# Performance work log

Measured on AMD Instinct MI355X. Metric: run time of the kernel, lower is better.

Reference implementation:

```python
import jax, jax.numpy as jnp
import numpy as np

B, C, L = 64, 64, 8192
EPS = float(np.finfo(np.float32).eps)  # matches np.finfo(np.float32).eps in the torch code


def setup_inputs() -> dict:
    key = jax.random.key(0)
    k1, k2, k3 = jax.random.split(key, 3)
    data = jax.random.normal(k1, (B, C, L), dtype=jnp.float32)
    idxes = jax.random.randint(k2, (B, L), 0, L).astype(jnp.int32)
    # prefix lengths in [1, L] so every slice is non-empty (ragged branch)
    zero_pos = jax.random.randint(k3, (B,), 1, L + 1)
    return {"data": data, "idxes": idxes, "zero_pos": zero_pos}


def reference(data, idxes, zero_pos):
    # data: [B, C, L]; per-batch mean/std over the prefix data[b, :, :zero_pos[b]]
    Bn, Cn, Ln = data.shape
    mask = (jnp.arange(Ln)[None, :] < zero_pos[:, None])[:, None, :].astype(data.dtype)  # [B,1,L]
    cnt = Cn * zero_pos.astype(data.dtype)  # [B] number of elements in each prefix
    mean = jnp.sum(data * mask, axis=(1, 2)) / cnt  # [B]
    diff = (data - mean[:, None, None]) * mask  # [B,C,L]
    var = jnp.sum(diff * diff, axis=(1, 2)) / (cnt - 1.0)  # unbiased, as torch.std
    std = jnp.sqrt(var)  # [B]
    out = (data - mean[:, None, None]) / (std[:, None, None] + EPS)
    return (out, idxes, zero_pos)
```

## Files before the change

kernel.cpp:

```cpp
#include <hip/hip_runtime.h>
#include <hip/hip_bf16.h>
#include <math.h>

#define BB 64
#define CC 64
#define LL 8192
#define EPS_F 1.1920928955078125e-07f
#define STATS_SPLITS 16


__global__ void tln_stats(const float* __restrict__ data,
                          const int* __restrict__ zero_pos,
                          float* __restrict__ sums) {
    const int b = blockIdx.x;
    const int s = blockIdx.y;
    const int tid = threadIdx.x;
    const int zp = zero_pos[b];
    const int nv = zp >> 2;
    const float* base = data + (size_t)b * CC * LL;

    float sum = 0.0f, sq = 0.0f;
    for (int c = s; c < CC; c += STATS_SPLITS) {
        const float* rowp = base + (size_t)c * LL;
        const float4* row4 = (const float4*)rowp;
        for (int i = tid; i < nv; i += 256) {
            float4 v = row4[i];
            sum += v.x + v.y + v.z + v.w;
            sq  += v.x * v.x + v.y * v.y + v.z * v.z + v.w * v.w;
        }
        for (int l = (nv << 2) + tid; l < zp; l += 256) {
            float v = rowp[l];
            sum += v;
            sq  += v * v;
        }
    }

    #pragma unroll
    for (int off = 32; off > 0; off >>= 1) {
        sum += __shfl_down(sum, off);
        sq  += __shfl_down(sq, off);
    }
    __shared__ float lsum[4], lsq[4];
    const int wave = tid >> 6;
    const int lane = tid & 63;
    if (lane == 0) { lsum[wave] = sum; lsq[wave] = sq; }
    __syncthreads();
    if (tid == 0) {
        float ts = lsum[0] + lsum[1] + lsum[2] + lsum[3];
        float tq = lsq[0] + lsq[1] + lsq[2] + lsq[3];
        atomicAdd(&sums[2 * b],     ts);
        atomicAdd(&sums[2 * b + 1], tq);
    }
}

__global__ void tln_finalize(const float* __restrict__ sums,
                             const int* __restrict__ zero_pos,
                             float* __restrict__ mean_inv) {
    const int b = threadIdx.x;
    if (b >= BB) return;
    const float cnt = (float)CC * (float)zero_pos[b];
    const float mean = sums[2 * b] / cnt;
    const float var = (sums[2 * b + 1] - cnt * mean * mean) / (cnt - 1.0f);
    const float stdv = sqrtf(var);
    mean_inv[2 * b]     = mean;
    mean_inv[2 * b + 1] = 1.0f / (stdv + EPS_F);
}

__global__ void tln_normalize(const float4* __restrict__ data,
                              const float* __restrict__ mean_inv,
                              float4* __restrict__ out) {
    const size_t i = (size_t)blockIdx.x * blockDim.x + threadIdx.x;
    const int b = (int)(i >> 17);
    const float m   = mean_inv[2 * b];
    const float inv = mean_inv[2 * b + 1];
    float4 v = data[i];
    float4 o;
    o.x = (v.x - m) * inv;
    o.y = (v.y - m) * inv;
    o.z = (v.z - m) * inv;
    o.w = (v.w - m) * inv;
    out[i] = o;
}

__global__ void tln_aux(const int4* __restrict__ idxes,
                        const int* __restrict__ zero_pos,
                        float4* __restrict__ out_idx,
                        float* __restrict__ out_zp) {
    const int i = blockIdx.x * blockDim.x + threadIdx.x;
    const int n4 = (BB * LL) / 4;
    if (i < n4) {
        int4 v = idxes[i];
        float4 o;
        o.x = (float)v.x; o.y = (float)v.y; o.z = (float)v.z; o.w = (float)v.w;
        out_idx[i] = o;
    }
    if (i < BB) out_zp[i] = (float)zero_pos[i];
}

extern "C" void kernel_launch(void* const* d_in, const int* in_sizes, int n_in,
                              void* d_out, int out_size, void* d_ws, size_t ws_size,
                              hipStream_t stream) {
    const float* data    = (const float*)d_in[0];
    const int* idxes     = (const int*)d_in[1];
    const int* zero_pos  = (const int*)d_in[2];

    float* sums     = (float*)d_ws;
    float* mean_inv = sums + 2 * BB;

    float* out_data = (float*)d_out;
    float* out_idx  = out_data + (size_t)BB * CC * LL;
    float* out_zp   = out_idx + (size_t)BB * LL;

    hipMemsetAsync(d_ws, 0, 2 * BB * sizeof(float), stream);

    tln_stats<<<dim3(BB, STATS_SPLITS), 256, 0, stream>>>(data, zero_pos, sums);
    tln_finalize<<<1, 64, 0, stream>>>(sums, zero_pos, mean_inv);

    const size_t nvec = (size_t)BB * CC * LL / 4;
    tln_normalize<<<(unsigned)(nvec / 256), 256, 0, stream>>>(
        (const float4*)data, mean_inv, (float4*)out_data);

    const int n4 = (BB * LL) / 4;
    tln_aux<<<(n4 + 255) / 256, 256, 0, stream>>>(
        (const int4*)idxes, zero_pos, (float4*)out_idx, out_zp);
}
```

Baseline: 253.9 us.

## Fuse finalize and aux into normalize kernel, replace atomics with partials

Stats blocks now write per-split partial sums instead of atomically accumulating, removing the memset. Each normalize block reduces the partials for its batch into shared mean/inv-std, eliminating the separate finalize kernel. The idx/zero_pos conversion is appended as extra blocks of the same launch, and stats splits double for more parallelism. This trades launch overhead for a small redundant reduction and a barrier in every normalize block.

```diff
diff --git a/kernel.cpp b/kernel.cpp
--- a/kernel.cpp
+++ b/kernel.cpp
@@ -6,12 +6,14 @@
 #define CC 64
 #define LL 8192
 #define EPS_F 1.1920928955078125e-07f
-#define STATS_SPLITS 16
+#define SPLITS 32
+#define NB_NORM 32768
+#define NB_AUX  512
 
 
 __global__ void tln_stats(const float* __restrict__ data,
                           const int* __restrict__ zero_pos,
-                          float* __restrict__ sums) {
+                          float2* __restrict__ partials) {
     const int b = blockIdx.x;
     const int s = blockIdx.y;
     const int tid = threadIdx.x;
@@ -20,7 +22,7 @@
     const float* base = data + (size_t)b * CC * LL;
 
     float sum = 0.0f, sq = 0.0f;
-    for (int c = s; c < CC; c += STATS_SPLITS) {
+    for (int c = s; c < CC; c += SPLITS) {
         const float* rowp = base + (size_t)c * LL;
         const float4* row4 = (const float4*)rowp;
         for (int i = tid; i < nv; i += 256) {
@@ -46,55 +48,64 @@
     if (lane == 0) { lsum[wave] = sum; lsq[wave] = sq; }
     __syncthreads();
     if (tid == 0) {
-        float ts = lsum[0] + lsum[1] + lsum[2] + lsum[3];
-        float tq = lsq[0] + lsq[1] + lsq[2] + lsq[3];
-        atomicAdd(&sums[2 * b],     ts);
-        atomicAdd(&sums[2 * b + 1], tq);
+        float2 p;
+        p.x = lsum[0] + lsum[1] + lsum[2] + lsum[3];
+        p.y = lsq[0] + lsq[1] + lsq[2] + lsq[3];
+        partials[b * SPLITS + s] = p;
     }
 }
 
-__global__ void tln_finalize(const float* __restrict__ sums,
-                             const int* __restrict__ zero_pos,
-                             float* __restrict__ mean_inv) {
-    const int b = threadIdx.x;
-    if (b >= BB) return;
-    const float cnt = (float)CC * (float)zero_pos[b];
-    const float mean = sums[2 * b] / cnt;
-    const float var = (sums[2 * b + 1] - cnt * mean * mean) / (cnt - 1.0f);
-    const float stdv = sqrtf(var);
-    mean_inv[2 * b]     = mean;
-    mean_inv[2 * b + 1] = 1.0f / (stdv + EPS_F);
-}
+__global__ void tln_fused(const float4* __restrict__ data4,
+                          const float2* __restrict__ partials,
+                          const int* __restrict__ zero_pos,
+                          const int4* __restrict__ idxes,
+                          float4* __restrict__ out4,
+                          float4* __restrict__ out_idx,
+                          float* __restrict__ out_zp) {
+    const int blk = blockIdx.x;
+    const int tid = threadIdx.x;
 
-__global__ void tln_normalize(const float4* __restrict__ data,
-                              const float* __restrict__ mean_inv,
-                              float4* __restrict__ out) {
-    const size_t i = (size_t)blockIdx.x * blockDim.x + threadIdx.x;
-    const int b = (int)(i >> 17);
-    const float m   = mean_inv[2 * b];
-    const float inv = mean_inv[2 * b + 1];
-    float4 v = data[i];
-    float4 o;
-    o.x = (v.x - m) * inv;
-    o.y = (v.y - m) * inv;
-    o.z = (v.z - m) * inv;
-    o.w = (v.w - m) * inv;
-    out[i] = o;
-}
-
-__global__ void tln_aux(const int4* __restrict__ idxes,
-                        const int* __restrict__ zero_pos,
-                        float4* __restrict__ out_idx,
-                        float* __restrict__ out_zp) {
-    const int i = blockIdx.x * blockDim.x + threadIdx.x;
-    const int n4 = (BB * LL) / 4;
-    if (i < n4) {
+    if (blk < NB_NORM) {
+        const int b = blk >> 9;
+        __shared__ float s_m, s_inv;
+        if (tid < 64) {
+            float s_ = 0.0f, q_ = 0.0f;
+            if (tid < SPLITS) {
+                float2 p = partials[b * SPLITS + tid];
+                s_ = p.x; q_ = p.y;
+            }
+            #pragma unroll
+            for (int off = 16; off > 0; off >>= 1) {
+                s_ += __shfl_down(s_, off);
+                q_ += __shfl_down(q_, off);
+            }
+            if (tid == 0) {
+                const float cnt = (float)CC * (float)zero_pos[b];
+                const float mean = s_ / cnt;
+                const float var = (q_ - cnt * mean * mean) / (cnt - 1.0f);
+                s_m = mean;
+                s_inv = 1.0f / (sqrtf(var) + EPS_F);
+            }
+        }
+        __syncthreads();
+        const float m = s_m, inv = s_inv;
+        const size_t i = (size_t)blk * 256 + tid;
+        float4 v = data4[i];
+        float4 o;
+        o.x = (v.x - m) * inv;
+        o.y = (v.y - m) * inv;
+        o.z = (v.z - m) * inv;
+        o.w = (v.w - m) * inv;
+        out4[i] = o;
+    } else {
+        const int j = blk - NB_NORM;
+        const int i = j * 256 + tid;
         int4 v = idxes[i];
         float4 o;
         o.x = (float)v.x; o.y = (float)v.y; o.z = (float)v.z; o.w = (float)v.w;
         out_idx[i] = o;
+        if (j == 0 && tid < BB) out_zp[tid] = (float)zero_pos[tid];
     }
-    if (i < BB) out_zp[i] = (float)zero_pos[i];
 }
 
 extern "C" void kernel_launch(void* const* d_in, const int* in_sizes, int n_in,
@@ -104,23 +115,15 @@
     const int* idxes     = (const int*)d_in[1];
     const int* zero_pos  = (const int*)d_in[2];
 
-    float* sums     = (float*)d_ws;
-    float* mean_inv = sums + 2 * BB;
+    float2* partials = (float2*)d_ws;
 
     float* out_data = (float*)d_out;
     float* out_idx  = out_data + (size_t)BB * CC * LL;
     float* out_zp   = out_idx + (size_t)BB * LL;
 
-    hipMemsetAsync(d_ws, 0, 2 * BB * sizeof(float), stream);
+    tln_stats<<<dim3(BB, SPLITS), 256, 0, stream>>>(data, zero_pos, partials);
 
-    tln_stats<<<dim3(BB, STATS_SPLITS), 256, 0, stream>>>(data, zero_pos, sums);
-    tln_finalize<<<1, 64, 0, stream>>>(sums, zero_pos, mean_inv);
-
-    const size_t nvec = (size_t)BB * CC * LL / 4;
-    tln_normalize<<<(unsigned)(nvec / 256), 256, 0, stream>>>(
-        (const float4*)data, mean_inv, (float4*)out_data);
-
-    const int n4 = (BB * LL) / 4;
-    tln_aux<<<(n4 + 255) / 256, 256, 0, stream>>>(
-        (const int4*)idxes, zero_pos, (float4*)out_idx, out_zp);
+    tln_fused<<<NB_NORM + NB_AUX, 256, 0, stream>>>(
+        (const float4*)data, partials, zero_pos, (const int4*)idxes,
+        (float4*)out_data, (float4*)out_idx, out_zp);
 }
```

New measurement: 251.0 us. No clear change (-1.1%).
